# Kernel tuning notes

Hardware: AMD Instinct MI355X
Metric: run time of the kernel (lower is better)

Reference implementation:

```python
import jax, jax.numpy as jnp
import numpy as np
import math

STEM = 64
TOK = 128
RADIUS = 0.16
K = 32


def sinusoidal_pos_emb_3d(x, dim):
    # x: [..., 3] -> [..., dim]; dim/3 channels per axis (half sin, half cos)
    per_axis = dim // 3
    half = per_axis // 2
    scale = math.log(10000.0) / (half - 1)
    freqs = jnp.exp(-scale * jnp.arange(half, dtype=x.dtype))  # [half]
    ang = x[..., :, None] * freqs  # [..., 3, half]
    emb = jnp.concatenate([jnp.sin(ang), jnp.cos(ang)], axis=-1)  # [..., 3, per_axis]
    return emb.reshape(*x.shape[:-1], dim)


def query_ball_point(radius, nsample, xyz):
    # xyz: [B, N, 3] -> idx [B, N, nsample] int32
    B, N, _ = xyz.shape
    d2 = jnp.sum((xyz[:, :, None, :] - xyz[:, None, :, :]) ** 2, axis=-1)  # [B,N,N]
    cand = jnp.where(d2 <= radius * radius, jnp.arange(N, dtype=jnp.int32)[None, None, :], N)
    idx = jnp.sort(cand, axis=-1)[..., :nsample]  # first nsample in-ball indices
    first = idx[..., :1]  # self is always in-ball (d=0), so first is valid
    return jnp.where(idx == N, first, idx)


def index_points(points, idx):
    # points [B,N,C], idx [B,S,K] -> [B,S,K,C]
    return jax.vmap(lambda p, i: p[i])(points, idx)


def point_mlp(x, W, b, activate):
    y = x @ W + b
    return jax.nn.relu(y) if activate else y


def setup_inputs() -> dict:
    key = jax.random.key(0)
    ks = jax.random.split(key, 10)
    B, N = 2, 4096
    xyz = jax.random.uniform(ks[0], (B, N, 3), dtype=jnp.float32)
    point_feature = jax.random.normal(ks[1], (B, N, STEM), dtype=jnp.float32)
    c_in = STEM + 3 + 24 + 96  # 187
    def lin(k, i, o):
        s = 1.0 / np.sqrt(i)
        return jax.random.uniform(k, (i, o), jnp.float32, -s, s)
    W1 = lin(ks[2], c_in, TOK); b1 = jnp.zeros((TOK,), jnp.float32)
    W2 = lin(ks[3], TOK, TOK); b2 = jnp.zeros((TOK,), jnp.float32)
    W3 = lin(ks[4], TOK, TOK); b3 = jnp.zeros((TOK,), jnp.float32)
    W4 = lin(ks[5], TOK, TOK); b4 = jnp.zeros((TOK,), jnp.float32)
    return {"xyz": xyz, "point_feature": point_feature,
            "W1": W1, "b1": b1, "W2": W2, "b2": b2,
            "W3": W3, "b3": b3, "W4": W4, "b4": b4}


def reference(xyz, point_feature, W1, b1, W2, b2, W3, b3, W4, b4):
    idx = query_ball_point(RADIUS, K, xyz)                 # [B,N,K]
    grouped_xyz = index_points(xyz, idx)                   # [B,N,K,3]
    grouped_feature = index_points(point_feature, idx)     # [B,N,K,STEM]
    relative_xyz = grouped_xyz - xyz[:, :, None, :]        # [B,N,K,3]
    rel_pe = sinusoidal_pos_emb_3d(relative_xyz, 24)       # [B,N,K,24]
    abs_pe = sinusoidal_pos_emb_3d(xyz, 96)                # [B,N,96]
    abs_pe = jnp.broadcast_to(abs_pe[:, :, None, :], (*idx.shape, 96))
    grouped_input = jnp.concatenate(
        [grouped_feature, relative_xyz, rel_pe, abs_pe], axis=-1)  # [B,N,K,187]
    h = point_mlp(grouped_input, W1, b1, True)
    h = point_mlp(h, W2, b2, False)                        # [B,N,K,TOK]
    scene_point_feature = jnp.max(h, axis=2)               # [B,N,TOK]
    g = jnp.max(scene_point_feature, axis=1, keepdims=True)  # [B,1,TOK]
    g = point_mlp(g, W3, b3, True)
    return point_mlp(g, W4, b4, False)                     # [B,1,TOK]
```

## Files before the change

### kernel.cpp

```cpp
#include <hip/hip_runtime.h>
#include <stdint.h>

#define BATCH 2
#define NPTS  4096
#define KNBR  32
#define TOKC  128

typedef _Float16 half8 __attribute__((ext_vector_type(8)));
typedef _Float16 half4 __attribute__((ext_vector_type(4)));
typedef float    f32x4 __attribute__((ext_vector_type(4)));

#define OFF_FH    (1u << 20)
#define OFF_AH    (3u << 20)
#define OFF_W1F   ((5u << 20) + 2048)
#define OFF_W2F   ((5u << 20) + 10240)
#define OFF_BMAX  (6u << 20)
#define OFF_BMAX2 (8u << 20)

#define NMAIN 4096

__global__ __launch_bounds__(256) void k_pre(const float* __restrict__ xyz,
                                             const float* __restrict__ feat,
                                             const float* __restrict__ W1,
                                             const float* __restrict__ W2,
                                             const float* __restrict__ b1,
                                             int* __restrict__ oidx,
                                             _Float16* __restrict__ Fh,
                                             _Float16* __restrict__ Ah,
                                             _Float16* __restrict__ W1F,
                                             _Float16* __restrict__ W2F) {
    __shared__ __align__(16) _Float16 inL[16][168];
    const int t = threadIdx.x;
    const int w = t >> 6, lane = t & 63;

    if (blockIdx.x < 2048) {
        int wave = blockIdx.x * 4 + w;
        int b = wave >> 12;
        int n = wave & (NPTS - 1);
        const float* xb = xyz + (size_t)b * NPTS * 3;
        float cx = xb[n * 3 + 0], cy = xb[n * 3 + 1], cz = xb[n * 3 + 2];
        const float R2 = 0.0256f;
        int cnt = 0;
        int first = 0;
        int* out = oidx + (size_t)wave * KNBR;
        float px = xb[lane * 3 + 0], py = xb[lane * 3 + 1], pz = xb[lane * 3 + 2];
        for (int base = 0; base < NPTS; base += 64) {
            #pragma clang fp contract(off)
            float dx = px - cx, dy = py - cy, dz = pz - cz;
            float d2 = (dx * dx + dy * dy) + dz * dz;
            bool hit = d2 <= R2;
            int jn = ((base + 64) & (NPTS - 1)) + lane;
            float nx = xb[jn * 3 + 0], ny = xb[jn * 3 + 1], nz = xb[jn * 3 + 2];
            unsigned long long m = __ballot(hit);
            if (cnt == 0 && m) first = base + (int)__builtin_ctzll(m);
            if (hit) {
                int pos = cnt + (int)__popcll(m & ((1ull << lane) - 1ull));
                if (pos < KNBR) out[pos] = base + lane;
            }
            cnt += (int)__popcll(m);
            if (cnt >= KNBR) break;
            px = nx; py = ny; pz = nz;
        }
        if (lane >= cnt && lane < KNBR) out[lane] = first;
        return;
    }

    if (blockIdx.x >= 2560) {
        int f = blockIdx.x - 2560;
        #pragma unroll
        for (int s = 0; s < 2; s++) {
            int e = t + s * 256;
            int ln = e >> 3, j = e & 7;
            int l15 = ln & 15, g = ln >> 4;
            if (f < 8) {
                int k = g * 8 + j;
                int c = f * 16 + l15;
                float val = (k < 27) ? W1[(64 + k) * TOKC + c] : 0.f;
                W1F[f * 512 + e] = (_Float16)val;
            } else {
                int f2 = f - 8;
                int ct = f2 >> 2, kc = f2 & 3;
                int k = kc * 32 + g * 8 + j;
                int c = ct * 16 + l15;
                W2F[f2 * 512 + e] = (_Float16)W2[k * TOKC + c];
            }
        }
        return;
    }

    const int l15 = lane & 15, g = lane >> 4;
    const int g0 = (blockIdx.x - 2048) * 16;

    half8 af[2][2];
    half8 ap[2][3];
    float4 b1v[2];
    #pragma unroll
    for (int rt = 0; rt < 2; rt++) {
        int c = 32 * w + 16 * rt + l15;
        #pragma unroll
        for (int kc = 0; kc < 2; kc++)
            #pragma unroll
            for (int j = 0; j < 8; j++)
                af[rt][kc][j] = (_Float16)W1[(kc * 32 + g * 8 + j) * TOKC + c];
        #pragma unroll
        for (int kc = 0; kc < 3; kc++)
            #pragma unroll
            for (int j = 0; j < 8; j++)
                ap[rt][kc][j] = (_Float16)W1[(91 + kc * 32 + g * 8 + j) * TOKC + c];
        b1v[rt] = *(const float4*)&b1[32 * w + 16 * rt + g * 4];
    }

    {
        float4 v = ((const float4*)(feat + (size_t)g0 * 64))[t];
        half4 hv = {(_Float16)v.x, (_Float16)v.y, (_Float16)v.z, (_Float16)v.w};
        *(half4*)&inL[t >> 4][(t & 15) * 4] = hv;
    }
    {
        int p = t >> 4, v0 = (t & 15) * 6;
        const float* xp = xyz + (size_t)(g0 + p) * 3;
        #pragma unroll
        for (int u = 0; u < 6; u++) {
            int d = v0 + u;
            int a = d >> 5, i = d & 31, fi = i & 15;
            float fr = __expf(-0.6140226914650789f * (float)fi);
            float ang = xp[a] * fr;
            inL[p][64 + d] = (_Float16)((i < 16) ? __sinf(ang) : __cosf(ang));
        }
    }
    __syncthreads();

    f32x4 cF[2], cA[2];
    #pragma unroll
    for (int rt = 0; rt < 2; rt++) { f32x4 z = {0.f, 0.f, 0.f, 0.f}; cF[rt] = z; cA[rt] = z; }
    #pragma unroll
    for (int kc = 0; kc < 2; kc++) {
        half8 bx = *(const half8*)&inL[l15][kc * 32 + g * 8];
        cF[0] = __builtin_amdgcn_mfma_f32_16x16x32_f16(af[0][kc], bx, cF[0], 0, 0, 0);
        cF[1] = __builtin_amdgcn_mfma_f32_16x16x32_f16(af[1][kc], bx, cF[1], 0, 0, 0);
    }
    #pragma unroll
    for (int kc = 0; kc < 3; kc++) {
        half8 bx = *(const half8*)&inL[l15][64 + kc * 32 + g * 8];
        cA[0] = __builtin_amdgcn_mfma_f32_16x16x32_f16(ap[0][kc], bx, cA[0], 0, 0, 0);
        cA[1] = __builtin_amdgcn_mfma_f32_16x16x32_f16(ap[1][kc], bx, cA[1], 0, 0, 0);
    }

    size_t pbase = ((size_t)g0 + l15) * TOKC;
    #pragma unroll
    for (int rt = 0; rt < 2; rt++) {
        int ch0 = 32 * w + 16 * rt + g * 4;
        half4 fv, av;
        #pragma unroll
        for (int r = 0; r < 4; r++) {
            fv[r] = (_Float16)cF[rt][r];
            av[r] = (_Float16)(cA[rt][r] + b1v[rt][r]);
        }
        *(half4*)&Fh[pbase + ch0] = fv;
        *(half4*)&Ah[pbase + ch0] = av;
    }
}

__global__ __launch_bounds__(256, 2) void k_main(const float* __restrict__ xyz,
                                                 const int* __restrict__ idxw,
                                                 const _Float16* __restrict__ Fh,
                                                 const _Float16* __restrict__ Ah,
                                                 const _Float16* __restrict__ W1F,
                                                 const _Float16* __restrict__ W2F,
                                                 float* __restrict__ bmax) {
    __shared__ __align__(16) _Float16 xinL[64 * 40];
    __shared__ __align__(16) _Float16 hfa[64 * 136];
    __shared__ __align__(16) _Float16 arowL[256];
    __shared__ int jidxL[64];

    const int t = threadIdx.x;
    const int w = t >> 6, lane = t & 63;
    const int l15 = lane & 15, g = lane >> 4;
    const int b = blockIdx.x >> 11;
    const int n0 = (blockIdx.x & 2047) * 2;
    const size_t gp0 = (size_t)b * NPTS + n0;
    const float* xb = xyz + (size_t)b * NPTS * 3;

    half8 a1[2];
    half8 a2[2][4];
    #pragma unroll
    for (int rt = 0; rt < 2; rt++) {
        a1[rt] = *(const half8*)&W1F[(2 * w + rt) * 512 + lane * 8];
        #pragma unroll
        for (int kc = 0; kc < 4; kc++)
            a2[rt][kc] = *(const half8*)&W2F[((2 * w + rt) * 4 + kc) * 512 + lane * 8];
    }

    if (t < 64) jidxL[t] = idxw[gp0 * KNBR + t];
    ((ushort*)arowL)[t] = ((const ushort*)(Ah + gp0 * TOKC))[t];
    __syncthreads();

    const float FR[4] = {1.f, 0.0464158883f, 0.00215443469f, 1e-4f};
    {
        int p = t >> 2, q = t & 3;
        int j = jidxL[p];
        const half8* frp = (const half8*)(Fh + ((size_t)b * NPTS + j) * TOKC + q * 32);
        half8 fb[4];
        #pragma unroll
        for (int i = 0; i < 4; i++) fb[i] = frp[i];
        const half8* arp = (const half8*)(arowL + (p >> 5) * TOKC + q * 32);
        half8* dst = (half8*)(hfa + p * 136 + q * 32);
        #pragma unroll
        for (int i = 0; i < 4; i++) dst[i] = fb[i] + arp[i];
    }
    if (t < 128) {
        int p = t >> 1, hh = t & 1;
        int n = n0 + (p >> 5), j = jidxL[p];
        float rx = xb[j * 3 + 0] - xb[n * 3 + 0];
        float ry = xb[j * 3 + 1] - xb[n * 3 + 1];
        float rz = xb[j * 3 + 2] - xb[n * 3 + 2];
        float v[16];
        if (hh == 0) {
            v[0] = rx; v[1] = ry; v[2] = rz;
            #pragma unroll
            for (int fi = 0; fi < 4; fi++) {
                float ang = rx * FR[fi];
                v[3 + fi] = __sinf(ang);
                v[7 + fi] = __cosf(ang);
            }
            #pragma unroll
            for (int fi = 0; fi < 4; fi++) v[11 + fi] = __sinf(ry * FR[fi]);
            v[15] = __cosf(ry * FR[0]);
        } else {
            #pragma unroll
            for (int fi = 1; fi < 4; fi++) v[fi - 1] = __cosf(ry * FR[fi]);
            #pragma unroll
            for (int fi = 0; fi < 4; fi++) {
                float ang = rz * FR[fi];
                v[3 + fi] = __sinf(ang);
                v[7 + fi] = __cosf(ang);
            }
            #pragma unroll
            for (int i = 11; i < 16; i++) v[i] = 0.f;
        }
        half8 h0, h1;
        #pragma unroll
        for (int i = 0; i < 8; i++) { h0[i] = (_Float16)v[i]; h1[i] = (_Float16)v[8 + i]; }
        *(half8*)&xinL[p * 40 + hh * 16]     = h0;
        *(half8*)&xinL[p * 40 + hh * 16 + 8] = h1;
    }
    __syncthreads();

    #pragma unroll
    for (int ct = 0; ct < 4; ct++) {
        int p = ct * 16 + l15;
        half8 bx = *(const half8*)&xinL[p * 40 + g * 8];
        f32x4 z = {0.f, 0.f, 0.f, 0.f};
        f32x4 c1a = __builtin_amdgcn_mfma_f32_16x16x32_f16(a1[0], bx, z, 0, 0, 0);
        f32x4 c1b = __builtin_amdgcn_mfma_f32_16x16x32_f16(a1[1], bx, z, 0, 0, 0);
        #pragma unroll
        for (int rt = 0; rt < 2; rt++) {
            int ch0 = 32 * w + 16 * rt + g * 4;
            half4* hp = (half4*)&hfa[p * 136 + ch0];
            half4 bias = *hp;
            f32x4 cc = rt ? c1b : c1a;
            half4 hv;
            #pragma unroll
            for (int r = 0; r < 4; r++) {
                float s = cc[r] + (float)bias[r];
                hv[r] = (_Float16)fmaxf(s, 0.f);
            }
            *hp = hv;
        }
    }
    __syncthreads();

    f32x4 c2[4][2];
    #pragma unroll
    for (int ct = 0; ct < 4; ct++)
        #pragma unroll
        for (int rt = 0; rt < 2; rt++) {
            f32x4 z = {0.f, 0.f, 0.f, 0.f};
            c2[ct][rt] = z;
        }
    #pragma unroll
    for (int kc = 0; kc < 4; kc++) {
        #pragma unroll
        for (int ct = 0; ct < 4; ct++) {
            half8 bx = *(const half8*)&hfa[(ct * 16 + l15) * 136 + kc * 32 + g * 8];
            c2[ct][0] = __builtin_amdgcn_mfma_f32_16x16x32_f16(a2[0][kc], bx, c2[ct][0], 0, 0, 0);
            c2[ct][1] = __builtin_amdgcn_mfma_f32_16x16x32_f16(a2[1][kc], bx, c2[ct][1], 0, 0, 0);
        }
    }
    float mx[2][4];
    #pragma unroll
    for (int rt = 0; rt < 2; rt++)
        #pragma unroll
        for (int r = 0; r < 4; r++)
            mx[rt][r] = fmaxf(fmaxf(c2[0][rt][r], c2[1][rt][r]), fmaxf(c2[2][rt][r], c2[3][rt][r]));

    #pragma unroll
    for (int rt = 0; rt < 2; rt++)
        #pragma unroll
        for (int r = 0; r < 4; r++)
            #pragma unroll
            for (int off = 1; off < 16; off <<= 1)
                mx[rt][r] = fmaxf(mx[rt][r], __shfl_xor(mx[rt][r], off));

    if (l15 == 0) {
        float* brow = bmax + (size_t)blockIdx.x * TOKC;
        float4 v0 = make_float4(mx[0][0], mx[0][1], mx[0][2], mx[0][3]);
        float4 v1 = make_float4(mx[1][0], mx[1][1], mx[1][2], mx[1][3]);
        *(float4*)&brow[32 * w + g * 4]      = v0;
        *(float4*)&brow[32 * w + 16 + g * 4] = v1;
    }
}

__global__ __launch_bounds__(256) void k_red(const float* __restrict__ bmax,
                                             float* __restrict__ bmax2) {
    __shared__ float red[256];
    const int i = blockIdx.x, t = threadIdx.x;
    const int c = t & 127, h = t >> 7;
    const float* base = bmax + ((size_t)i * 32 + (size_t)h * 16) * TOKC + c;
    float m = -1e30f;
    #pragma unroll
    for (int k = 0; k < 16; k++) m = fmaxf(m, base[(size_t)k * TOKC]);
    red[t] = m;
    __syncthreads();
    if (t < 128) bmax2[(size_t)i * TOKC + t] = fmaxf(red[t], red[t + 128]);
}

__global__ __launch_bounds__(256) void k_tail(const float* __restrict__ bmax2,
                                              const float* __restrict__ b2,
                                              const float* __restrict__ W3,
                                              const float* __restrict__ b3,
                                              const float* __restrict__ W4,
                                              const float* __restrict__ b4,
                                              float* __restrict__ out) {
    __shared__ float red[256];
    __shared__ float gl[128], sl[128];
    const int b = blockIdx.x, t = threadIdx.x;
    const int c = t & 127, h = t >> 7;
    const float* base = bmax2 + ((size_t)b * 64 + (size_t)h * 32) * TOKC + c;
    float m = -1e30f;
    #pragma unroll
    for (int k = 0; k < 32; k++) m = fmaxf(m, base[(size_t)k * TOKC]);
    red[t] = m;
    __syncthreads();
    if (t < 128) gl[t] = fmaxf(red[t], red[t + 128]) + b2[t];
    __syncthreads();
    if (t < 128) {
        float s = b3[t];
        for (int k = 0; k < 128; k++) s += gl[k] * W3[k * TOKC + t];
        sl[t] = fmaxf(s, 0.f);
    }
    __syncthreads();
    if (t < 128) {
        float o = b4[t];
        for (int k = 0; k < 128; k++) o += sl[k] * W4[k * TOKC + t];
        out[b * TOKC + t] = o;
    }
}

extern "C" void kernel_launch(void* const* d_in, const int* in_sizes, int n_in,
                              void* d_out, int out_size, void* d_ws, size_t ws_size,
                              hipStream_t stream) {
    const float* xyz  = (const float*)d_in[0];
    const float* feat = (const float*)d_in[1];
    const float* W1   = (const float*)d_in[2];
    const float* b1   = (const float*)d_in[3];
    const float* W2   = (const float*)d_in[4];
    const float* b2   = (const float*)d_in[5];
    const float* W3   = (const float*)d_in[6];
    const float* b3   = (const float*)d_in[7];
    const float* W4   = (const float*)d_in[8];
    const float* b4   = (const float*)d_in[9];

    char* ws = (char*)d_ws;
    int*          idxw  = (int*)ws;
    _Float16*     Fh    = (_Float16*)(ws + OFF_FH);
    _Float16*     Ah    = (_Float16*)(ws + OFF_AH);
    _Float16*     W1F   = (_Float16*)(ws + OFF_W1F);
    _Float16*     W2F   = (_Float16*)(ws + OFF_W2F);
    float*        bmax  = (float*)(ws + OFF_BMAX);
    float*        bmax2 = (float*)(ws + OFF_BMAX2);

    k_pre<<<dim3(2600), dim3(256), 0, stream>>>(xyz, feat, W1, W2, b1,
                                                idxw, Fh, Ah, W1F, W2F);
    k_main<<<dim3(NMAIN), dim3(256), 0, stream>>>(xyz, idxw, Fh, Ah, W1F, W2F, bmax);
    k_red<<<dim3(128), dim3(256), 0, stream>>>(bmax, bmax2);
    k_tail<<<dim3(BATCH), dim3(256), 0, stream>>>(bmax2, b2, W3, b3, W4, b4, (float*)d_out);
}
```

Before: 138.8 us.

## Process eight points per k_main block with prefetch; drop ball-query early exit

k_main now loops over four pairs of points per block, with a quarter as many blocks. It keeps a running max in registers and prefetches the next pair's neighbor indices and Ah row. This amortizes the weight-fragment loads and the per-block output writes, and the reduction kernels are resized to match. The ball query drops the early break and the software prefetch, so every query scans all 4096 points. That adds substantial work to k_pre, and the occupancy hint is raised to 3 blocks per SIMD, which may constrain registers.

```diff
diff --git a/kernel.cpp b/kernel.cpp
--- a/kernel.cpp
+++ b/kernel.cpp
@@ -15,9 +15,9 @@
 #define OFF_W1F   ((5u << 20) + 2048)
 #define OFF_W2F   ((5u << 20) + 10240)
 #define OFF_BMAX  (6u << 20)
-#define OFF_BMAX2 (8u << 20)
-
-#define NMAIN 4096
+#define OFF_BMAX2 (7u << 20)
+
+#define NMAIN 1024
 
 __global__ __launch_bounds__(256) void k_pre(const float* __restrict__ xyz,
                                              const float* __restrict__ feat,
@@ -43,23 +43,20 @@
         int cnt = 0;
         int first = 0;
         int* out = oidx + (size_t)wave * KNBR;
-        float px = xb[lane * 3 + 0], py = xb[lane * 3 + 1], pz = xb[lane * 3 + 2];
         for (int base = 0; base < NPTS; base += 64) {
             #pragma clang fp contract(off)
+            int j = base + lane;
+            float px = xb[j * 3 + 0], py = xb[j * 3 + 1], pz = xb[j * 3 + 2];
             float dx = px - cx, dy = py - cy, dz = pz - cz;
             float d2 = (dx * dx + dy * dy) + dz * dz;
             bool hit = d2 <= R2;
-            int jn = ((base + 64) & (NPTS - 1)) + lane;
-            float nx = xb[jn * 3 + 0], ny = xb[jn * 3 + 1], nz = xb[jn * 3 + 2];
             unsigned long long m = __ballot(hit);
             if (cnt == 0 && m) first = base + (int)__builtin_ctzll(m);
             if (hit) {
                 int pos = cnt + (int)__popcll(m & ((1ull << lane) - 1ull));
-                if (pos < KNBR) out[pos] = base + lane;
+                if (pos < KNBR) out[pos] = j;
             }
             cnt += (int)__popcll(m);
-            if (cnt >= KNBR) break;
-            px = nx; py = ny; pz = nz;
         }
         if (lane >= cnt && lane < KNBR) out[lane] = first;
         return;
@@ -160,7 +157,7 @@
     }
 }
 
-__global__ __launch_bounds__(256, 2) void k_main(const float* __restrict__ xyz,
+__global__ __launch_bounds__(256, 3) void k_main(const float* __restrict__ xyz,
                                                  const int* __restrict__ idxw,
                                                  const _Float16* __restrict__ Fh,
                                                  const _Float16* __restrict__ Ah,
@@ -175,9 +172,8 @@
     const int t = threadIdx.x;
     const int w = t >> 6, lane = t & 63;
     const int l15 = lane & 15, g = lane >> 4;
-    const int b = blockIdx.x >> 11;
-    const int n0 = (blockIdx.x & 2047) * 2;
-    const size_t gp0 = (size_t)b * NPTS + n0;
+    const int b = blockIdx.x >> 9;
+    const int pbase = (blockIdx.x & 511) * 8;
     const float* xb = xyz + (size_t)b * NPTS * 3;
 
     half8 a1[2];
@@ -190,121 +186,149 @@
             a2[rt][kc] = *(const half8*)&W2F[((2 * w + rt) * 4 + kc) * 512 + lane * 8];
     }
 
-    if (t < 64) jidxL[t] = idxw[gp0 * KNBR + t];
-    ((ushort*)arowL)[t] = ((const ushort*)(Ah + gp0 * TOKC))[t];
-    __syncthreads();
+    float mxAll[2][4];
+    #pragma unroll
+    for (int rt = 0; rt < 2; rt++)
+        #pragma unroll
+        for (int r = 0; r < 4; r++) mxAll[rt][r] = -1e30f;
 
     const float FR[4] = {1.f, 0.0464158883f, 0.00215443469f, 1e-4f};
+
+    int jreg = 0;
+    ushort ar0;
     {
-        int p = t >> 2, q = t & 3;
-        int j = jidxL[p];
-        const half8* frp = (const half8*)(Fh + ((size_t)b * NPTS + j) * TOKC + q * 32);
-        half8 fb[4];
-        #pragma unroll
-        for (int i = 0; i < 4; i++) fb[i] = frp[i];
-        const half8* arp = (const half8*)(arowL + (p >> 5) * TOKC + q * 32);
-        half8* dst = (half8*)(hfa + p * 136 + q * 32);
-        #pragma unroll
-        for (int i = 0; i < 4; i++) dst[i] = fb[i] + arp[i];
-    }
-    if (t < 128) {
-        int p = t >> 1, hh = t & 1;
-        int n = n0 + (p >> 5), j = jidxL[p];
-        float rx = xb[j * 3 + 0] - xb[n * 3 + 0];
-        float ry = xb[j * 3 + 1] - xb[n * 3 + 1];
-        float rz = xb[j * 3 + 2] - xb[n * 3 + 2];
-        float v[16];
-        if (hh == 0) {
-            v[0] = rx; v[1] = ry; v[2] = rz;
-            #pragma unroll
-            for (int fi = 0; fi < 4; fi++) {
-                float ang = rx * FR[fi];
-                v[3 + fi] = __sinf(ang);
-                v[7 + fi] = __cosf(ang);
-            }
-            #pragma unroll
-            for (int fi = 0; fi < 4; fi++) v[11 + fi] = __sinf(ry * FR[fi]);
-            v[15] = __cosf(ry * FR[0]);
-        } else {
-            #pragma unroll
-            for (int fi = 1; fi < 4; fi++) v[fi - 1] = __cosf(ry * FR[fi]);
-            #pragma unroll
-            for (int fi = 0; fi < 4; fi++) {
-                float ang = rz * FR[fi];
-                v[3 + fi] = __sinf(ang);
-                v[7 + fi] = __cosf(ang);
-            }
-            #pragma unroll
-            for (int i = 11; i < 16; i++) v[i] = 0.f;
-        }
-        half8 h0, h1;
-        #pragma unroll
-        for (int i = 0; i < 8; i++) { h0[i] = (_Float16)v[i]; h1[i] = (_Float16)v[8 + i]; }
-        *(half8*)&xinL[p * 40 + hh * 16]     = h0;
-        *(half8*)&xinL[p * 40 + hh * 16 + 8] = h1;
-    }
-    __syncthreads();
-
-    #pragma unroll
-    for (int ct = 0; ct < 4; ct++) {
-        int p = ct * 16 + l15;
-        half8 bx = *(const half8*)&xinL[p * 40 + g * 8];
-        f32x4 z = {0.f, 0.f, 0.f, 0.f};
-        f32x4 c1a = __builtin_amdgcn_mfma_f32_16x16x32_f16(a1[0], bx, z, 0, 0, 0);
-        f32x4 c1b = __builtin_amdgcn_mfma_f32_16x16x32_f16(a1[1], bx, z, 0, 0, 0);
-        #pragma unroll
-        for (int rt = 0; rt < 2; rt++) {
-            int ch0 = 32 * w + 16 * rt + g * 4;
-            half4* hp = (half4*)&hfa[p * 136 + ch0];
-            half4 bias = *hp;
-            f32x4 cc = rt ? c1b : c1a;
-            half4 hv;
+        const size_t gq = (size_t)b * NPTS + pbase;
+        if (t < 64) jreg = idxw[gq * KNBR + t];
+        ar0 = ((const ushort*)(Ah + gq * TOKC))[t];
+    }
+
+    for (int it = 0; it < 4; it++) {
+        const int n0 = pbase + it * 2;
+        const size_t gp0 = (size_t)b * NPTS + n0;
+
+        if (t < 64) jidxL[t] = jreg;
+        ((ushort*)arowL)[t] = ar0;
+        __syncthreads();
+
+        if (it < 3) {
+            const size_t gq = gp0 + 2;
+            if (t < 64) jreg = idxw[gq * KNBR + t];
+            ar0 = ((const ushort*)(Ah + gq * TOKC))[t];
+        }
+
+        {
+            int p = t >> 2, q = t & 3;
+            int j = jidxL[p];
+            const half8* frp = (const half8*)(Fh + ((size_t)b * NPTS + j) * TOKC + q * 32);
+            half8 fb[4];
+            #pragma unroll
+            for (int i = 0; i < 4; i++) fb[i] = frp[i];
+            const half8* arp = (const half8*)(arowL + (p >> 5) * TOKC + q * 32);
+            half8* dst = (half8*)(hfa + p * 136 + q * 32);
+            #pragma unroll
+            for (int i = 0; i < 4; i++) dst[i] = fb[i] + arp[i];
+        }
+        if (t < 128) {
+            int p = t >> 1, hh = t & 1;
+            int n = n0 + (p >> 5), j = jidxL[p];
+            float rx = xb[j * 3 + 0] - xb[n * 3 + 0];
+            float ry = xb[j * 3 + 1] - xb[n * 3 + 1];
+            float rz = xb[j * 3 + 2] - xb[n * 3 + 2];
+            float v[16];
+            if (hh == 0) {
+                v[0] = rx; v[1] = ry; v[2] = rz;
+                #pragma unroll
+                for (int fi = 0; fi < 4; fi++) {
+                    float ang = rx * FR[fi];
+                    v[3 + fi] = __sinf(ang);
+                    v[7 + fi] = __cosf(ang);
+                }
+                #pragma unroll
+                for (int fi = 0; fi < 4; fi++) v[11 + fi] = __sinf(ry * FR[fi]);
+                v[15] = __cosf(ry * FR[0]);
+            } else {
+                #pragma unroll
+                for (int fi = 1; fi < 4; fi++) v[fi - 1] = __cosf(ry * FR[fi]);
+                #pragma unroll
+                for (int fi = 0; fi < 4; fi++) {
+                    float ang = rz * FR[fi];
+                    v[3 + fi] = __sinf(ang);
+                    v[7 + fi] = __cosf(ang);
+                }
+                #pragma unroll
+                for (int i = 11; i < 16; i++) v[i] = 0.f;
+            }
+            half8 h0, h1;
+            #pragma unroll
+            for (int i = 0; i < 8; i++) { h0[i] = (_Float16)v[i]; h1[i] = (_Float16)v[8 + i]; }
+            *(half8*)&xinL[p * 40 + hh * 16]     = h0;
+            *(half8*)&xinL[p * 40 + hh * 16 + 8] = h1;
+        }
+        __syncthreads();
+
+        #pragma unroll
+        for (int ct = 0; ct < 4; ct++) {
+            int p = ct * 16 + l15;
+            half8 bx = *(const half8*)&xinL[p * 40 + g * 8];
+            f32x4 z = {0.f, 0.f, 0.f, 0.f};
+            f32x4 c1a = __builtin_amdgcn_mfma_f32_16x16x32_f16(a1[0], bx, z, 0, 0, 0);
+            f32x4 c1b = __builtin_amdgcn_mfma_f32_16x16x32_f16(a1[1], bx, z, 0, 0, 0);
+            #pragma unroll
+            for (int rt = 0; rt < 2; rt++) {
+                int ch0 = 32 * w + 16 * rt + g * 4;
+                half4* hp = (half4*)&hfa[p * 136 + ch0];
+                half4 bias = *hp;
+                f32x4 cc = rt ? c1b : c1a;
+                half4 hv;
+                #pragma unroll
+                for (int r = 0; r < 4; r++) {
+                    float s = cc[r] + (float)bias[r];
+                    hv[r] = (_Float16)fmaxf(s, 0.f);
+                }
+                *hp = hv;
+            }
+        }
+        __syncthreads();
+
+        f32x4 c2[4][2];
+        #pragma unroll
+        for (int ct = 0; ct < 4; ct++)
+            #pragma unroll
+            for (int rt = 0; rt < 2; rt++) {
+                f32x4 z = {0.f, 0.f, 0.f, 0.f};
+                c2[ct][rt] = z;
+            }
+        #pragma unroll
+        for (int kc = 0; kc < 4; kc++) {
+            #pragma unroll
+            for (int ct = 0; ct < 4; ct++) {
+                half8 bx = *(const half8*)&hfa[(ct * 16 + l15) * 136 + kc * 32 + g * 8];
+                c2[ct][0] = __builtin_amdgcn_mfma_f32_16x16x32_f16(a2[0][kc], bx, c2[ct][0], 0, 0, 0);
+                c2[ct][1] = __builtin_amdgcn_mfma_f32_16x16x32_f16(a2[1][kc], bx, c2[ct][1], 0, 0, 0);
+            }
+        }
+        #pragma unroll
+        for (int rt = 0; rt < 2; rt++)
             #pragma unroll
             for (int r = 0; r < 4; r++) {
-                float s = cc[r] + (float)bias[r];
-                hv[r] = (_Float16)fmaxf(s, 0.f);
-            }
-            *hp = hv;
-        }
-    }
-    __syncthreads();
-
-    f32x4 c2[4][2];
-    #pragma unroll
-    for (int ct = 0; ct < 4; ct++)
-        #pragma unroll
-        for (int rt = 0; rt < 2; rt++) {
-            f32x4 z = {0.f, 0.f, 0.f, 0.f};
-            c2[ct][rt] = z;
-        }
-    #pragma unroll
-    for (int kc = 0; kc < 4; kc++) {
-        #pragma unroll
-        for (int ct = 0; ct < 4; ct++) {
-            half8 bx = *(const half8*)&hfa[(ct * 16 + l15) * 136 + kc * 32 + g * 8];
-            c2[ct][0] = __builtin_amdgcn_mfma_f32_16x16x32_f16(a2[0][kc], bx, c2[ct][0], 0, 0, 0);
-            c2[ct][1] = __builtin_amdgcn_mfma_f32_16x16x32_f16(a2[1][kc], bx, c2[ct][1], 0, 0, 0);
-        }
-    }
-    float mx[2][4];
+                float m0 = fmaxf(fmaxf(c2[0][rt][r], c2[1][rt][r]), fmaxf(c2[2][rt][r], c2[3][rt][r]));
+                mxAll[rt][r] = fmaxf(mxAll[rt][r], m0);
+            }
+        __syncthreads();
+    }
+
     #pragma unroll
     for (int rt = 0; rt < 2; rt++)
         #pragma unroll
         for (int r = 0; r < 4; r++)
-            mx[rt][r] = fmaxf(fmaxf(c2[0][rt][r], c2[1][rt][r]), fmaxf(c2[2][rt][r], c2[3][rt][r]));
-
-    #pragma unroll
-    for (int rt = 0; rt < 2; rt++)
-        #pragma unroll
-        for (int r = 0; r < 4; r++)
             #pragma unroll
             for (int off = 1; off < 16; off <<= 1)
-                mx[rt][r] = fmaxf(mx[rt][r], __shfl_xor(mx[rt][r], off));
+                mxAll[rt][r] = fmaxf(mxAll[rt][r], __shfl_xor(mxAll[rt][r], off));
 
     if (l15 == 0) {
         float* brow = bmax + (size_t)blockIdx.x * TOKC;
-        float4 v0 = make_float4(mx[0][0], mx[0][1], mx[0][2], mx[0][3]);
-        float4 v1 = make_float4(mx[1][0], mx[1][1], mx[1][2], mx[1][3]);
+        float4 v0 = make_float4(mxAll[0][0], mxAll[0][1], mxAll[0][2], mxAll[0][3]);
+        float4 v1 = make_float4(mxAll[1][0], mxAll[1][1], mxAll[1][2], mxAll[1][3]);
         *(float4*)&brow[32 * w + g * 4]      = v0;
         *(float4*)&brow[32 * w + 16 + g * 4] = v1;
     }
@@ -315,10 +339,10 @@
     __shared__ float red[256];
     const int i = blockIdx.x, t = threadIdx.x;
     const int c = t & 127, h = t >> 7;
-    const float* base = bmax + ((size_t)i * 32 + (size_t)h * 16) * TOKC + c;
+    const float* base = bmax + ((size_t)i * 16 + (size_t)h * 8) * TOKC + c;
     float m = -1e30f;
     #pragma unroll
-    for (int k = 0; k < 16; k++) m = fmaxf(m, base[(size_t)k * TOKC]);
+    for (int k = 0; k < 8; k++) m = fmaxf(m, base[(size_t)k * TOKC]);
     red[t] = m;
     __syncthreads();
     if (t < 128) bmax2[(size_t)i * TOKC + t] = fmaxf(red[t], red[t + 128]);
@@ -335,10 +359,10 @@
     __shared__ float gl[128], sl[128];
     const int b = blockIdx.x, t = threadIdx.x;
     const int c = t & 127, h = t >> 7;
-    const float* base = bmax2 + ((size_t)b * 64 + (size_t)h * 32) * TOKC + c;
+    const float* base = bmax2 + ((size_t)b * 32 + (size_t)h * 16) * TOKC + c;
     float m = -1e30f;
     #pragma unroll
-    for (int k = 0; k < 32; k++) m = fmaxf(m, base[(size_t)k * TOKC]);
+    for (int k = 0; k < 16; k++) m = fmaxf(m, base[(size_t)k * TOKC]);
     red[t] = m;
     __syncthreads();
     if (t < 128) gl[t] = fmaxf(red[t], red[t + 128]) + b2[t];
@@ -382,6 +406,6 @@
     k_pre<<<dim3(2600), dim3(256), 0, stream>>>(xyz, feat, W1, W2, b1,
                                                 idxw, Fh, Ah, W1F, W2F);
     k_main<<<dim3(NMAIN), dim3(256), 0, stream>>>(xyz, idxw, Fh, Ah, W1F, W2F, bmax);
-    k_red<<<dim3(128), dim3(256), 0, stream>>>(bmax, bmax2);
+    k_red<<<dim3(64), dim3(256), 0, stream>>>(bmax, bmax2);
     k_tail<<<dim3(BATCH), dim3(256), 0, stream>>>(bmax2, b2, W3, b3, W4, b4, (float*)d_out);
 }
```

New measurement: 146.1 us. 1.05x slower.
